# Kernel optimization log

Measured on AMD Instinct MI355X. Metric: run time of the kernel, lower is better.

Reference implementation:

```python
import jax, jax.numpy as jnp
import numpy as np
from functools import partial

B, S, V, H, NH, NKV, M, L = 2, 2048, 51200, 1536, 24, 4, 8960, 8
DH = H // NH  # 64
EPS = 1e-6


def setup_inputs() -> dict:
    key = jax.random.key(0)
    ks = jax.random.split(key, 16)
    sc = 0.02
    w = lambda k, shape: jax.random.normal(k, shape, jnp.float32) * sc
    inp = {
        "input_ids": jax.random.randint(ks[0], (B, S), 0, V),
        "attention_mask": jnp.ones((B, S), jnp.float32),
        "embed": w(ks[1], (V, H)),
        "Wq": w(ks[2], (L, H, H)),          "bq": jnp.zeros((L, H), jnp.float32),
        "Wk": w(ks[3], (L, H, NKV * DH)),   "bk": jnp.zeros((L, NKV * DH), jnp.float32),
        "Wv": w(ks[4], (L, H, NKV * DH)),   "bv": jnp.zeros((L, NKV * DH), jnp.float32),
        "Wo": w(ks[5], (L, H, H)),
        "ln1": jnp.ones((L, H), jnp.float32),
        "ln2": jnp.ones((L, H), jnp.float32),
        "Wg": w(ks[6], (L, H, M)),
        "Wu": w(ks[7], (L, H, M)),
        "Wd": w(ks[8], (L, M, H)),
        "norm_w": jnp.ones((H,), jnp.float32),
        "W1": w(ks[9], (H, H)), "b1": jnp.zeros((H,), jnp.float32),
        "W2": w(ks[10], (H, 1)), "b2": jnp.zeros((1,), jnp.float32),
    }
    inv_freq = 1.0 / (10000.0 ** (jnp.arange(0, DH, 2, dtype=jnp.float32) / DH))
    freqs = jnp.outer(jnp.arange(S, dtype=jnp.float32), inv_freq)  # [S, DH/2]
    emb = jnp.concatenate([freqs, freqs], axis=-1)                 # [S, DH]
    inp["cos"] = jnp.cos(emb)
    inp["sin"] = jnp.sin(emb)
    return inp


def _rms(x, w):
    var = jnp.mean(x.astype(jnp.float32) ** 2, axis=-1, keepdims=True)
    return w * (x * jax.lax.rsqrt(var + EPS)).astype(x.dtype)


def _rotate_half(x):
    x1, x2 = jnp.split(x, 2, axis=-1)
    return jnp.concatenate([-x2, x1], axis=-1)


def _forward(input_ids, attention_mask, embed, Wq, bq, Wk, bk, Wv, bv, Wo,
             ln1, ln2, Wg, Wu, Wd, norm_w, W1, b1, W2, b2, cos, sin):
    scale = 1.0 / np.sqrt(DH)
    b, s = input_ids.shape
    c = cos[None, :s, None, :]  # [1,S,1,DH]
    sn = sin[None, :s, None, :]
    rope = lambda t: t * c + _rotate_half(t) * sn
    mask0 = attention_mask[:, None, None, :] == 0  # [B,1,1,S]

    def block(x, p):
        wq, bq_, wk, bk_, wv, bv_, wo, ln1w, ln2w, wg, wu, wd = p
        h = _rms(x, ln1w)
        q = (h @ wq + bq_).reshape(b, s, NH, DH)
        k = (h @ wk + bk_).reshape(b, s, NKV, DH)
        v = (h @ wv + bv_).reshape(b, s, NKV, DH)
        q, k = rope(q), rope(k)
        k = jnp.repeat(k, NH // NKV, axis=2)  # GQA expand to NH heads
        v = jnp.repeat(v, NH // NKV, axis=2)
        scores = jnp.einsum('bqhd,bkhd->bhqk', q, k) * scale
        scores = jnp.where(mask0, -1e10, scores)
        probs = jax.nn.softmax(scores, axis=-1)  # dropout: eval mode (identity)
        attn = jnp.einsum('bhqk,bkhd->bqhd', probs, v).reshape(b, s, H)
        x = x + attn @ wo
        h = _rms(x, ln2w)
        x = x + (jax.nn.sigmoid(h @ wg) * (h @ wu)) @ wd
        return x, None

    x = embed[input_ids]  # [B,S,H]
    x, _ = jax.lax.scan(block, x, (Wq, bq, Wk, bk, Wv, bv, Wo, ln1, ln2, Wg, Wu, Wd))
    x = _rms(x, norm_w)
    h = jax.nn.gelu(x @ W1 + b1, approximate=False)  # torch nn.GELU default = exact
    return h @ W2 + b2  # [B,S,1]


def reference(input_ids, attention_mask, embed, Wq, bq, Wk, bk, Wv, bv, Wo,
              ln1, ln2, Wg, Wu, Wd, norm_w, W1, b1, W2, b2, cos, sin):
    return _forward(input_ids, attention_mask, embed, Wq, bq, Wk, bk, Wv, bv, Wo,
                    ln1, ln2, Wg, Wu, Wd, norm_w, W1, b1, W2, b2, cos, sin)
```

## Files before the change

kernel.cpp:

```cpp
#include <hip/hip_runtime.h>

typedef float f32x4 __attribute__((ext_vector_type(4)));
typedef short s16x8 __attribute__((ext_vector_type(8)));
typedef unsigned short u16;
typedef unsigned short u16x4 __attribute__((ext_vector_type(4)));
typedef unsigned short u16x8 __attribute__((ext_vector_type(8)));
typedef unsigned int u32x2 __attribute__((ext_vector_type(2)));

__device__ __forceinline__ float bf2f(u16 u){ union{unsigned int i; float f;} v; v.i=((unsigned int)u)<<16; return v.f; }
__device__ __forceinline__ u16 f2bf(float f){ union{float f; unsigned int i;} v; v.f=f; return (u16)((v.i + 0x7FFFu + ((v.i>>16)&1u))>>16); }
__device__ __forceinline__ float aexp2(float x){ float r; asm("v_exp_f32 %0, %1" : "=v"(r) : "v"(x)); return r; }
__device__ __forceinline__ unsigned int cvtpk(float lo, float hi){ unsigned int r; asm("v_cvt_pk_bf16_f32 %0, %1, %2" : "=v"(r) : "v"(lo), "v"(hi)); return r; }

#define LOG2E 1.44269504089f

__device__ __forceinline__ void gld16(const void* gp, void* lp){
  __builtin_amdgcn_global_load_lds((__attribute__((address_space(1))) void*)(void*)gp,
                                   (__attribute__((address_space(3))) void*)lp, 16, 0, 0);
}

__device__ __forceinline__ void job_map(int bid, int gridx, int nrt, int nct, int ksplit,
                                        int SR, int SC, int& rt, int& ct, int& ks){
  int jpx = gridx >> 3;
  int wgid = (bid & 7)*jpx + (bid >> 3);
  int nj1 = nrt*nct;
  ks = wgid / nj1; int rr = wgid - ks*nj1;
  int spc = SR*SC, nstc = nct/SC;
  int st = rr / spc, win = rr - st*spc;
  int str_ = st / nstc, stc = st - str_*nstc;
  int wr = win / SC, wc = win - wr*SC;
  rt = str_*SR + wr;
  ct = stc*SC + wc;
}

__global__ __launch_bounds__(256) void k_embed(const int* __restrict__ ids, const float* __restrict__ emb, float* __restrict__ x){
  int r = blockIdx.x;
  int id = ids[r];
  const f32x4* src = (const f32x4*)(emb + (size_t)id*1536);
  f32x4* dst = (f32x4*)(x + (size_t)r*1536);
  for (int i = threadIdx.x; i < 384; i += 256) dst[i] = src[i];
}

__global__ __launch_bounds__(256) void k_mask(const float* __restrict__ mask, u16* __restrict__ mtab){
  int i = blockIdx.x*256 + threadIdx.x;
  float mv = mask[i];
  mtab[i] = (mv==0.f) ? f2bf(-1.4e9f) : f2bf(-4.f*LOG2E);
}

__global__ __launch_bounds__(256) void k_rms(const float* __restrict__ x, const float* __restrict__ w, u16* __restrict__ h){
  int r = blockIdx.x, tid = threadIdx.x;
  const f32x4* xr = (const f32x4*)(x + (size_t)r*1536);
  f32x4 v0 = xr[tid];
  float ss = v0.x*v0.x + v0.y*v0.y + v0.z*v0.z + v0.w*v0.w;
  f32x4 v1 = {0,0,0,0};
  if (tid < 128){ v1 = xr[256+tid]; ss += v1.x*v1.x + v1.y*v1.y + v1.z*v1.z + v1.w*v1.w; }
  #pragma unroll
  for (int off=32; off; off>>=1) ss += __shfl_xor(ss, off, 64);
  __shared__ float red[4];
  if ((tid&63)==0) red[tid>>6] = ss;
  __syncthreads();
  float tot = red[0]+red[1]+red[2]+red[3];
  float invr = rsqrtf(tot*(1.f/1536.f) + 1e-6f);
  const f32x4* w4 = (const f32x4*)w;
  u16x4* h4 = (u16x4*)(h + (size_t)r*1536);
  {
    f32x4 wv = w4[tid];
    u16x4 o; o.x=f2bf(v0.x*invr*wv.x); o.y=f2bf(v0.y*invr*wv.y); o.z=f2bf(v0.z*invr*wv.z); o.w=f2bf(v0.w*invr*wv.w);
    h4[tid] = o;
  }
  if (tid < 128){
    f32x4 wv = w4[256+tid];
    u16x4 o; o.x=f2bf(v1.x*invr*wv.x); o.y=f2bf(v1.y*invr*wv.y); o.z=f2bf(v1.z*invr*wv.z); o.w=f2bf(v1.w*invr*wv.w);
    h4[256+tid] = o;
  }
}

__global__ __launch_bounds__(256) void k_rms_add(float* __restrict__ x, const float* __restrict__ P, const float* __restrict__ w, u16* __restrict__ h){
  int r = blockIdx.x, tid = threadIdx.x;
  f32x4* xr = (f32x4*)(x + (size_t)r*1536);
  const f32x4* pr = (const f32x4*)(P + (size_t)r*1536);
  f32x4 v0 = xr[tid], p0 = pr[tid];
  v0.x+=p0.x; v0.y+=p0.y; v0.z+=p0.z; v0.w+=p0.w;
  xr[tid] = v0;
  float ss = v0.x*v0.x + v0.y*v0.y + v0.z*v0.z + v0.w*v0.w;
  f32x4 v1 = {0,0,0,0};
  if (tid < 128){
    v1 = xr[256+tid]; f32x4 p1 = pr[256+tid];
    v1.x+=p1.x; v1.y+=p1.y; v1.z+=p1.z; v1.w+=p1.w;
    xr[256+tid] = v1;
    ss += v1.x*v1.x + v1.y*v1.y + v1.z*v1.z + v1.w*v1.w;
  }
  #pragma unroll
  for (int off=32; off; off>>=1) ss += __shfl_xor(ss, off, 64);
  __shared__ float red[4];
  if ((tid&63)==0) red[tid>>6] = ss;
  __syncthreads();
  float tot = red[0]+red[1]+red[2]+red[3];
  float invr = rsqrtf(tot*(1.f/1536.f) + 1e-6f);
  const f32x4* w4 = (const f32x4*)w;
  u16x4* h4 = (u16x4*)(h + (size_t)r*1536);
  {
    f32x4 wv = w4[tid];
    u16x4 o; o.x=f2bf(v0.x*invr*wv.x); o.y=f2bf(v0.y*invr*wv.y); o.z=f2bf(v0.z*invr*wv.z); o.w=f2bf(v0.w*invr*wv.w);
    h4[tid] = o;
  }
  if (tid < 128){
    f32x4 wv = w4[256+tid];
    u16x4 o; o.x=f2bf(v1.x*invr*wv.x); o.y=f2bf(v1.y*invr*wv.y); o.z=f2bf(v1.z*invr*wv.z); o.w=f2bf(v1.w*invr*wv.w);
    h4[256+tid] = o;
  }
}

__device__ __forceinline__ void cvt_tile(const float* src, int K, int N, u16* dst, int k0, int n0, int roff, int mode){
  __shared__ float T[64*72];
  int tid = threadIdx.x;
  #pragma unroll
  for (int j=0;j<4;++j){
    int i = tid + j*256;
    int row = i>>4, nf = i&15;
    f32x4 vv = *(const f32x4*)(src + (size_t)(k0+row)*N + n0 + nf*4);
    *(f32x4*)&T[row*72 + nf*4] = vv;
  }
  __syncthreads();
  #pragma unroll
  for (int j=0;j<2;++j){
    int i = tid + j*256;
    int n = i>>3, kc = i&7;
    u16x8 o;
    #pragma unroll
    for (int m=0;m<8;++m) o[m] = f2bf(T[(kc*8+m)*72 + n]);
    int gn = n0 + n;
    int dr = (mode==0) ? (roff + gn) : (((gn>>4)<<5) + ((mode==2)?16:0) + (gn&15));
    *(u16x8*)(dst + (size_t)dr*K + k0 + kc*8) = o;
  }
}

__global__ __launch_bounds__(256) void k_cvt_layer(
  const float* __restrict__ Wq, const float* __restrict__ Wk, const float* __restrict__ Wv,
  const float* __restrict__ Wo, const float* __restrict__ Wg, const float* __restrict__ Wu,
  const float* __restrict__ Wd, u16* qkvt, u16* wot, u16* gut, u16* wdt)
{
  const float* src; int K, N; u16* dst; int roff=0, mode=0;
  switch (blockIdx.y){
    case 0: src=Wq; K=1536; N=1536; dst=qkvt; break;
    case 1: src=Wk; K=1536; N=256;  dst=qkvt; roff=1536; break;
    case 2: src=Wv; K=1536; N=256;  dst=qkvt; roff=1792; break;
    case 3: src=Wo; K=1536; N=1536; dst=wot;  break;
    case 4: src=Wg; K=1536; N=8960; dst=gut;  mode=1; break;
    case 5: src=Wu; K=1536; N=8960; dst=gut;  mode=2; break;
    default: src=Wd; K=8960; N=1536; dst=wdt; break;
  }
  int ntn = N>>6;
  int nt = (K>>6)*ntn;
  int t = blockIdx.x;
  if (t >= nt) return;
  cvt_tile(src, K, N, dst, (t/ntn)<<6, (t%ntn)<<6, roff, mode);
}

__global__ __launch_bounds__(256) void k_cvt_one(const float* __restrict__ src, u16* __restrict__ dst){
  int t = blockIdx.x;
  cvt_tile(src, 1536, 1536, dst, (t/24)<<6, (t%24)<<6, 0, 0);
}

#define MODE_QKV 0
#define MODE_WO 1
#define MODE_GATEUP 2
#define MODE_DOWN 3
#define MODE_W1 4

template<int MODE>
__global__ __launch_bounds__(256) void k_gemm(
  const u16* __restrict__ A, const u16* __restrict__ Bt, int K,
  int nrt, int nct, int ksplit, int klen, int SR, int SC,
  const float* __restrict__ bq_, const float* __restrict__ bk_, const float* __restrict__ bv_,
  float* __restrict__ xio, float* __restrict__ Pf,
  const float* __restrict__ cosT, const float* __restrict__ sinT,
  u16* __restrict__ o0, u16* __restrict__ o1, u16* __restrict__ o2)
{
  int rt, ct, ks;
  job_map(blockIdx.x, gridDim.x, nrt, nct, ksplit, SR, SC, rt, ct, ks);
  int kbase = ks*klen;
  int nt = klen >> 5;

  __shared__ __align__(16) u16 As[3][4096], Bs[3][4096];
  int tid = threadIdx.x;
  int lane = tid & 63, w = tid >> 6;
  int wr = w >> 1, wc = w & 1;
  int row0 = rt * 128, col0 = ct * 128;
  int l15 = lane & 15, l4 = lane >> 4;
  f32x4 acc[4][4] = {};
  const u16* aBase = A + (size_t)row0*K;
  const u16* bBase = Bt + (size_t)col0*K;
  int rr0 = tid & 127, kb0 = tid >> 7;
  int kb1 = kb0 + 2;

  auto stage = [&](int bf, int kt){
    gld16(aBase + (size_t)rr0*K + kt + kb0*8, &As[bf][tid*8]);
    gld16(bBase + (size_t)rr0*K + kt + kb0*8, &Bs[bf][tid*8]);
    gld16(aBase + (size_t)rr0*K + kt + kb1*8, &As[bf][(256+tid)*8]);
    gld16(bBase + (size_t)rr0*K + kt + kb1*8, &Bs[bf][(256+tid)*8]);
  };
  stage(0, kbase); stage(1, kbase+32);

  int bf = 0;
  for (int t = 0; t < nt; ++t){
    if (t < nt-1) asm volatile("s_waitcnt vmcnt(4)" ::: "memory");
    else          asm volatile("s_waitcnt vmcnt(0)" ::: "memory");
    __builtin_amdgcn_s_barrier();
    __builtin_amdgcn_sched_barrier(0);
    if (t+2 < nt){
      int nb = bf+2; if (nb >= 3) nb -= 3;
      stage(nb, kbase + (t+2)*32);
    }
    const u16* Ab = As[bf];
    const u16* Bb = Bs[bf];
    s16x8 af[4], bf_[4];
    #pragma unroll
    for (int i=0;i<4;++i) af[i]  = *(const s16x8*)&Ab[((l4<<7) + wr*64 + i*16 + l15)*8];
    #pragma unroll
    for (int jj=0;jj<4;++jj) bf_[jj] = *(const s16x8*)&Bb[((l4<<7) + wc*64 + jj*16 + l15)*8];
    __builtin_amdgcn_s_setprio(1);
    #pragma unroll
    for (int i=0;i<4;++i)
      #pragma unroll
      for (int jj=0;jj<4;++jj)
        acc[i][jj] = __builtin_amdgcn_mfma_f32_16x16x32_bf16(af[i], bf_[jj], acc[i][jj], 0, 0, 0);
    __builtin_amdgcn_s_setprio(0);
    if (++bf == 3) bf = 0;
  }

  #pragma unroll
  for (int i=0;i<4;++i)
    #pragma unroll
    for (int jj=0;jj<4;++jj)
      #pragma unroll
      for (int r=0;r<4;++r){
        int row = row0 + wr*64 + i*16 + l4*4 + r;
        int c   = col0 + wc*64 + jj*16 + l15;
        float v = acc[i][jj][r];
        if constexpr (MODE == MODE_QKV){
          int b = row >> 11, s = row & 2047;
          if (c < 1536){
            int d = c & 63, hd = c >> 6;
            float vv = v + bq_[c];
            float pv = acc[i][jj^2][r] + bq_[c^32];
            float cv = cosT[s*64+d], sv = sinT[s*64+d];
            float sgn = (d<32) ? -1.f : 1.f;
            float o = (vv*cv + sgn*pv*sv)*(0.125f*LOG2E);
            o0[(size_t)(b*24+hd)*131072 + (size_t)(s>>6)*4096
               + (s&63)*64 + (((d>>3)^(s&7))<<3) + (d&7)] = f2bf(o);
          } else if (c < 1792){
            int c2 = c - 1536, d = c2 & 63, kv = c2 >> 6;
            float vv = v + bk_[c2];
            float pv = acc[i][jj^2][r] + bk_[c2^32];
            float cv = cosT[s*64+d], sv = sinT[s*64+d];
            float sgn = (d<32) ? -1.f : 1.f;
            float o = vv*cv + sgn*pv*sv;
            o1[(size_t)(b*4+kv)*131072 + (size_t)(s>>6)*4096
               + (s&63)*64 + (((d>>3)^(s&7))<<3) + (d&7)] = f2bf(o);
          } else {
            int c2 = c - 1792, d = c2 & 63, kv = c2 >> 6;
            float vv = v + bv_[c2];
            o2[(size_t)(b*4+kv)*131072 + (size_t)(s>>6)*4096
               + d*64 + ((((s>>3)&7)^(d&7))<<3) + (s&7)] = f2bf(vv);
          }
        } else if constexpr (MODE == MODE_WO){
          xio[(size_t)row*1536 + c] += v;
        } else if constexpr (MODE == MODE_W1){
          v += bq_[c];
          float ge = 0.5f * v * (1.f + erff(v * 0.70710678118f));
          o0[(size_t)row*1536 + c] = f2bf(ge);
        }
      }
}

template<int MODE>
__global__ __launch_bounds__(512,2) void k_gemm256(
  const u16* __restrict__ A, const u16* __restrict__ Bt, int K,
  int nrt, int nct, int ksplit, int klen, int SR, int SC,
  float* __restrict__ xio, float* __restrict__ Pf, u16* __restrict__ o0)
{
  int rt, ct, ks;
  job_map(blockIdx.x, gridDim.x, nrt, nct, ksplit, SR, SC, rt, ct, ks);

  __shared__ __align__(16) u16 lds[2][2][16384];
  int tid = threadIdx.x;
  int lane = tid & 63, wid = tid >> 6;
  int wm = wid >> 2, wn = wid & 3;
  int l15 = lane & 15, l4 = lane >> 4;
  int lsw = l15 & 7;
  int row0 = rt*256, col0 = ct*256;
  int kbase = ks*klen*64;

  const u16* aB = A  + (size_t)row0*K + kbase;
  const u16* bB = Bt + (size_t)col0*K + kbase;
  int rsub = tid >> 3;
  int gsw  = (lane & 7) ^ ((lane >> 3) & 7);

  f32x4 acc[8][4] = {};

  auto sgA = [&](int bf, int kt, int c){
    gld16(aB + (size_t)(c*64 + rsub)*K + kt*64 + gsw*8, &lds[bf][0][(c*512+tid)*8]);
  };
  auto sgB = [&](int bf, int kt, int c){
    gld16(bB + (size_t)(c*64 + rsub)*K + kt*64 + gsw*8, &lds[bf][1][(c*512+tid)*8]);
  };

  sgB(0,0,0); sgB(0,0,1); sgB(0,0,2); sgB(0,0,3);
  sgA(0,0,0); sgA(0,0,2); sgA(0,0,1); sgA(0,0,3);

  for (int t = 0; t < klen; ++t){
    int b = t & 1, nb = b ^ 1;
    bool hn = (t+1 < klen);
    const u16* Ab = lds[b][0];
    const u16* Bb = lds[b][1];
    s16x8 bfr[4][2];

    asm volatile("s_waitcnt vmcnt(2)" ::: "memory");
    __builtin_amdgcn_s_barrier();
    __builtin_amdgcn_sched_barrier(0);
    {
      s16x8 af[2][2];
      #pragma unroll
      for (int ii=0;ii<2;++ii)
        #pragma unroll
        for (int ksu=0;ksu<2;++ksu)
          af[ii][ksu] = *(const s16x8*)&Ab[(wm*128 + ii*16 + l15)*64 + (((ksu*4+l4)^lsw)<<3)];
      #pragma unroll
      for (int j=0;j<4;++j)
        #pragma unroll
        for (int ksu=0;ksu<2;++ksu)
          bfr[j][ksu] = *(const s16x8*)&Bb[(wn*64 + j*16 + l15)*64 + (((ksu*4+l4)^lsw)<<3)];
      if (hn){ sgB(nb, t+1, 0); sgB(nb, t+1, 1); }
      asm volatile("s_waitcnt lgkmcnt(0)" ::: "memory");
      __builtin_amdgcn_sched_barrier(0);
      __builtin_amdgcn_s_setprio(1);
      #pragma unroll
      for (int ii=0;ii<2;++ii)
        #pragma unroll
        for (int j=0;j<4;++j)
          #pragma unroll
          for (int ksu=0;ksu<2;++ksu)
            acc[ii][j] = __builtin_amdgcn_mfma_f32_16x16x32_bf16(af[ii][ksu], bfr[j][ksu], acc[ii][j], 0,0,0);
      __builtin_amdgcn_s_setprio(0);
      __builtin_amdgcn_s_barrier();
    }
    {
      s16x8 af[2][2];
      #pragma unroll
      for (int ii=0;ii<2;++ii)
        #pragma unroll
        for (int ksu=0;ksu<2;++ksu)
          af[ii][ksu] = *(const s16x8*)&Ab[(wm*128 + 32 + ii*16 + l15)*64 + (((ksu*4+l4)^lsw)<<3)];
      if (hn){ sgB(nb, t+1, 2); sgB(nb, t+1, 3); }
      asm volatile("s_waitcnt lgkmcnt(0)" ::: "memory");
      __builtin_amdgcn_sched_barrier(0);
      __builtin_amdgcn_s_setprio(1);
      #pragma unroll
      for (int ii=0;ii<2;++ii)
        #pragma unroll
        for (int j=0;j<4;++j)
          #pragma unroll
          for (int ksu=0;ksu<2;++ksu)
            acc[2+ii][j] = __builtin_amdgcn_mfma_f32_16x16x32_bf16(af[ii][ksu], bfr[j][ksu], acc[2+ii][j], 0,0,0);
      __builtin_amdgcn_s_setprio(0);
      __builtin_amdgcn_s_barrier();
    }
    if (hn) asm volatile("s_waitcnt vmcnt(4)" ::: "memory");
    else    asm volatile("s_waitcnt vmcnt(0)" ::: "memory");
    __builtin_amdgcn_s_barrier();
    __builtin_amdgcn_sched_barrier(0);
    {
      s16x8 af[2][2];
      #pragma unroll
      for (int ii=0;ii<2;++ii)
        #pragma unroll
        for (int ksu=0;ksu<2;++ksu)
          af[ii][ksu] = *(const s16x8*)&Ab[(wm*128 + 64 + ii*16 + l15)*64 + (((ksu*4+l4)^lsw)<<3)];
      if (hn){ sgA(nb, t+1, 0); sgA(nb, t+1, 2); }
      asm volatile("s_waitcnt lgkmcnt(0)" ::: "memory");
      __builtin_amdgcn_sched_barrier(0);
      __builtin_amdgcn_s_setprio(1);
      #pragma unroll
      for (int ii=0;ii<2;++ii)
        #pragma unroll
        for (int j=0;j<4;++j)
          #pragma unroll
          for (int ksu=0;ksu<2;++ksu)
            acc[4+ii][j] = __builtin_amdgcn_mfma_f32_16x16x32_bf16(af[ii][ksu], bfr[j][ksu], acc[4+ii][j], 0,0,0);
      __builtin_amdgcn_s_setprio(0);
      __builtin_amdgcn_s_barrier();
    }
    {
      s16x8 af[2][2];
      #pragma unroll
      for (int ii=0;ii<2;++ii)
        #pragma unroll
        for (int ksu=0;ksu<2;++ksu)
          af[ii][ksu] = *(const s16x8*)&Ab[(wm*128 + 96 + ii*16 + l15)*64 + (((ksu*4+l4)^lsw)<<3)];
      if (hn){ sgA(nb, t+1, 1); sgA(nb, t+1, 3); }
      asm volatile("s_waitcnt lgkmcnt(0)" ::: "memory");
      __builtin_amdgcn_sched_barrier(0);
      __builtin_amdgcn_s_setprio(1);
      #pragma unroll
      for (int ii=0;ii<2;++ii)
        #pragma unroll
        for (int j=0;j<4;++j)
          #pragma unroll
          for (int ksu=0;ksu<2;++ksu)
            acc[6+ii][j] = __builtin_amdgcn_mfma_f32_16x16x32_bf16(af[ii][ksu], bfr[j][ksu], acc[6+ii][j], 0,0,0);
      __builtin_amdgcn_s_setprio(0);
      __builtin_amdgcn_s_barrier();
    }
  }

  if constexpr (MODE == MODE_GATEUP){
    #pragma unroll
    for (int i=0;i<8;++i)
      #pragma unroll
      for (int j2=0;j2<4;j2+=2)
        #pragma unroll
        for (int r=0;r<4;++r){
          int row = row0 + wm*128 + i*16 + l4*4 + r;
          int cp  = col0 + wn*64 + j2*16 + l15;
          float gv = acc[i][j2][r], uv = acc[i][j2+1][r];
          float sg = 1.f/(1.f + __expf(-gv));
          int n = ((cp>>5)<<4) + (cp&15);
          o0[(size_t)row*8960 + n] = f2bf(sg*uv);
        }
  } else {
    #pragma unroll
    for (int i=0;i<8;++i)
      #pragma unroll
      for (int j=0;j<4;++j)
        #pragma unroll
        for (int r=0;r<4;++r){
          int row = row0 + wm*128 + i*16 + l4*4 + r;
          int c   = col0 + wn*64 + j*16 + l15;
          float v = acc[i][j][r];
          if (ks == 0) Pf[(size_t)row*1536 + c] = v;
          else         xio[(size_t)row*1536 + c] += v;
        }
  }
}

__global__ __launch_bounds__(256) void k_attn(
  const u16* __restrict__ q, const u16* __restrict__ k, const u16* __restrict__ v,
  const u16* __restrict__ mtab, u16* __restrict__ attn)
{
  __shared__ __align__(16) u16 Qs[8192];
  __shared__ __align__(16) u16 Kd[2][4096];
  __shared__ __align__(16) u16 Vd[2][4096];
  int tid = threadIdx.x;
  int lane = tid & 63, w = tid >> 6;
  int qb = blockIdx.x;
  int bh = blockIdx.y;
  int b = bh / 24, hh = bh % 24, kv = hh / 6;
  int l15 = lane & 15, l4 = lane >> 4;
  int sw = l15 & 7;

  const u16* qhead = q + ((size_t)(b*24 + hh))*131072 + qb*8192;
  const u16* khead = k + ((size_t)(b*4  + kv))*131072;
  const u16* vhead = v + ((size_t)(b*4  + kv))*131072;
  const u16* mrow = mtab + b*2048;

  gld16(qhead + tid*8,        &Qs[tid*8]);
  gld16(qhead + (256+tid)*8,  &Qs[(256+tid)*8]);
  gld16(qhead + (512+tid)*8,  &Qs[(512+tid)*8]);
  gld16(qhead + (768+tid)*8,  &Qs[(768+tid)*8]);

  auto stage = [&](int bf, int kt){
    gld16(khead + kt*4096 + tid*8,       &Kd[bf][tid*8]);
    gld16(khead + kt*4096 + (256+tid)*8, &Kd[bf][(256+tid)*8]);
    gld16(vhead + kt*4096 + tid*8,       &Vd[bf][tid*8]);
    gld16(vhead + kt*4096 + (256+tid)*8, &Vd[bf][(256+tid)*8]);
  };
  stage(0, 0);

  s16x8 aq[2][2];
  f32x4 oacc[2][4] = {};
  float lsum[2] = {0.f, 0.f};
  u16* Pw = &Qs[w*2048];

  for (int t = 0; t < 32; ++t){
    asm volatile("s_waitcnt vmcnt(0)" ::: "memory");
    __builtin_amdgcn_s_barrier();
    __builtin_amdgcn_sched_barrier(0);
    if (t == 0){
      #pragma unroll
      for (int qa=0; qa<2; ++qa){
        int qrow = w*32 + qa*16 + l15;
        aq[qa][0] = *(const s16x8*)&Qs[qrow*64 + (( l4    ^ sw)<<3)];
        aq[qa][1] = *(const s16x8*)&Qs[qrow*64 + (((4+l4) ^ sw)<<3)];
      }
    }
    if (t+1 < 32) stage((t+1)&1, t+1);
    const u16* Kb = Kd[t&1];
    const u16* Vb = Vd[t&1];
    f32x4 sk[2][4] = {};
    __builtin_amdgcn_s_setprio(1);
    #pragma unroll
    for (int kn=0; kn<4; ++kn){
      int krow = kn*16 + l15;
      s16x8 a0 = *(const s16x8*)&Kb[krow*64 + (( l4    ^ sw)<<3)];
      s16x8 a1 = *(const s16x8*)&Kb[krow*64 + (((4+l4) ^ sw)<<3)];
      #pragma unroll
      for (int qa=0; qa<2; ++qa){
        sk[qa][kn] = __builtin_amdgcn_mfma_f32_16x16x32_bf16(a0, aq[qa][0], sk[qa][kn], 0,0,0);
        sk[qa][kn] = __builtin_amdgcn_mfma_f32_16x16x32_bf16(a1, aq[qa][1], sk[qa][kn], 0,0,0);
      }
    }
    __builtin_amdgcn_s_setprio(0);
    #pragma unroll
    for (int kn=0; kn<4; ++kn){
      u16x4 mv = *(const u16x4*)&mrow[t*64 + kn*16 + l4*4];
      #pragma unroll
      for (int qa=0; qa<2; ++qa){
        float p0 = aexp2(sk[qa][kn][0] + bf2f(mv.x));
        float p1 = aexp2(sk[qa][kn][1] + bf2f(mv.y));
        float p2 = aexp2(sk[qa][kn][2] + bf2f(mv.z));
        float p3 = aexp2(sk[qa][kn][3] + bf2f(mv.w));
        lsum[qa] += (p0 + p1) + (p2 + p3);
        u32x2 pk; pk.x = cvtpk(p0, p1); pk.y = cvtpk(p2, p3);
        int g = kn*2 + (l4>>1);
        *(u32x2*)&Pw[(qa*16 + l15)*64 + ((g ^ sw)<<3) + (l4&1)*4] = pk;
      }
    }
    __builtin_amdgcn_s_setprio(1);
    #pragma unroll
    for (int ksu=0; ksu<2; ++ksu){
      s16x8 bv[4];
      #pragma unroll
      for (int dg=0; dg<4; ++dg)
        bv[dg] = *(const s16x8*)&Vb[(dg*16+l15)*64 + (((ksu*4+l4) ^ sw)<<3)];
      #pragma unroll
      for (int qa=0; qa<2; ++qa){
        s16x8 ap = *(const s16x8*)&Pw[(qa*16 + l15)*64 + (((ksu*4+l4) ^ sw)<<3)];
        #pragma unroll
        for (int dg=0; dg<4; ++dg)
          oacc[qa][dg] = __builtin_amdgcn_mfma_f32_16x16x32_bf16(ap, bv[dg], oacc[qa][dg], 0,0,0);
      }
    }
    __builtin_amdgcn_s_setprio(0);
  }
  #pragma unroll
  for (int qa=0; qa<2; ++qa){
    float t2 = lsum[qa];
    t2 += __shfl_xor(t2, 16, 64);
    t2 += __shfl_xor(t2, 32, 64);
    float invq[4];
    #pragma unroll
    for (int r=0;r<4;++r) invq[r] = 1.f / __shfl(t2, l4*4 + r, 64);
    #pragma unroll
    for (int dg=0;dg<4;++dg)
      #pragma unroll
      for (int r=0;r<4;++r){
        int token = b*2048 + qb*128 + w*32 + qa*16 + l4*4 + r;
        int col = hh*64 + dg*16 + l15;
        attn[(size_t)token*1536 + col] = f2bf(oacc[qa][dg][r] * invq[r]);
      }
  }
}

__global__ __launch_bounds__(256) void k_gemv(const u16* __restrict__ h2, const float* __restrict__ W2, const float* __restrict__ b2, float* __restrict__ out){
  int tid = threadIdx.x, lane = tid & 63, w = tid >> 6;
  int r = blockIdx.x*4 + w;
  const u16* hr = h2 + (size_t)r*1536;
  float s = 0.f;
  #pragma unroll
  for (int i=0;i<24;++i){ int c = lane + i*64; s += bf2f(hr[c]) * W2[c]; }
  #pragma unroll
  for (int off=32; off; off>>=1) s += __shfl_xor(s, off, 64);
  if (lane == 0) out[r] = s + b2[0];
}

extern "C" void kernel_launch(void* const* d_in, const int* in_sizes, int n_in,
                              void* d_out, int out_size, void* d_ws, size_t ws_size,
                              hipStream_t stream)
{
  const int*   ids   = (const int*)d_in[0];
  const float* mask  = (const float*)d_in[1];
  const float* embed = (const float*)d_in[2];
  const float* Wq    = (const float*)d_in[3];
  const float* bq    = (const float*)d_in[4];
  const float* Wk    = (const float*)d_in[5];
  const float* bk    = (const float*)d_in[6];
  const float* Wv    = (const float*)d_in[7];
  const float* bv    = (const float*)d_in[8];
  const float* Wo    = (const float*)d_in[9];
  const float* ln1   = (const float*)d_in[10];
  const float* ln2   = (const float*)d_in[11];
  const float* Wg    = (const float*)d_in[12];
  const float* Wu    = (const float*)d_in[13];
  const float* Wd    = (const float*)d_in[14];
  const float* nw    = (const float*)d_in[15];
  const float* W1    = (const float*)d_in[16];
  const float* b1    = (const float*)d_in[17];
  const float* W2    = (const float*)d_in[18];
  const float* b2    = (const float*)d_in[19];
  const float* cosT  = (const float*)d_in[20];
  const float* sinT  = (const float*)d_in[21];

  char* ws = (char*)d_ws;
  float* x   = (float*)(ws + 0);
  u16* h     = (u16*)(ws + 25165824);
  u16* qb_   = (u16*)(ws + 37748736);
  u16* kb_   = (u16*)(ws + 50331648);
  u16* vb_   = (u16*)(ws + 52428800);
  u16* attn  = (u16*)(ws + 54525952);
  u16* g     = (u16*)(ws + 67108864);
  u16* qkvt  = (u16*)(ws + 140509184);
  u16* wot   = (u16*)(ws + 146800640);
  u16* gut   = (u16*)(ws + 151519232);
  u16* wdt   = (u16*)(ws + 206569472);
  u16* mtab  = (u16*)(ws + 234094592);
  float* Pf  = (float*)(ws + 37748736);
  (void)in_sizes; (void)n_in; (void)out_size; (void)ws_size;

  k_embed<<<4096, 256, 0, stream>>>(ids, embed, x);
  k_mask<<<16, 256, 0, stream>>>(mask, mtab);
  for (int l = 0; l < 8; ++l){
    k_cvt_layer<<<dim3(3360,7), 256, 0, stream>>>(
      Wq + (size_t)l*1536*1536, Wk + (size_t)l*1536*256, Wv + (size_t)l*1536*256,
      Wo + (size_t)l*1536*1536, Wg + (size_t)l*1536*8960, Wu + (size_t)l*1536*8960,
      Wd + (size_t)l*8960*1536, qkvt, wot, gut, wdt);
    if (l == 0) k_rms<<<4096, 256, 0, stream>>>(x, ln1, h);
    else        k_rms_add<<<4096, 256, 0, stream>>>(x, Pf, ln1 + l*1536, h);
    k_gemm<MODE_QKV><<<512, 256, 0, stream>>>(h, qkvt, 1536, 32, 16, 1, 1536, 8, 4,
        bq + l*1536, bk + l*256, bv + l*256, nullptr, nullptr, cosT, sinT, qb_, kb_, vb_);
    k_attn<<<dim3(16,48), 256, 0, stream>>>(qb_, kb_, vb_, mtab, attn);
    k_gemm<MODE_WO><<<384, 256, 0, stream>>>(attn, wot, 1536, 32, 12, 1, 1536, 8, 4,
        nullptr, nullptr, nullptr, x, nullptr, nullptr, nullptr, nullptr, nullptr, nullptr);
    k_rms<<<4096, 256, 0, stream>>>(x, ln2 + l*1536, h);
    k_gemm256<MODE_GATEUP><<<1120, 512, 0, stream>>>(h, gut, 1536, 16, 70, 1, 24, 8, 10,
        nullptr, nullptr, g);
    k_gemm256<MODE_DOWN><<<192, 512, 0, stream>>>(g, wdt, 8960, 16, 6, 2, 70, 4, 6,
        x, Pf, nullptr);
  }
  k_cvt_one<<<576, 256, 0, stream>>>(W1, wot);
  k_rms_add<<<4096, 256, 0, stream>>>(x, Pf, nw, h);
  k_gemm<MODE_W1><<<384, 256, 0, stream>>>(h, wot, 1536, 32, 12, 1, 1536, 8, 4,
      b1, nullptr, nullptr, nullptr, nullptr, nullptr, nullptr, attn, nullptr, nullptr);
  k_gemv<<<1024, 256, 0, stream>>>(attn, W2, b2, (float*)d_out);
}
```

Measured before the change: 5.128 ms.

## Batch rows per block in embed and RMSNorm kernels, store mask as fp32

The embedding gather now copies 8 rows per block, and the RMSNorm kernels handle 2 rows per 512-thread block, so far fewer, larger workgroups are launched. The mask table moves from bf16 to fp32, which removes the bf16-to-float conversion in the attention softmax loop at the cost of twice as many bytes per mask load. These kernels are small and memory-bound next to the GEMMs and attention, so the overall effect should be minor.

```diff
diff --git a/kernel.cpp b/kernel.cpp
--- a/kernel.cpp
+++ b/kernel.cpp
@@ -34,80 +34,92 @@
 }
 
 __global__ __launch_bounds__(256) void k_embed(const int* __restrict__ ids, const float* __restrict__ emb, float* __restrict__ x){
-  int r = blockIdx.x;
-  int id = ids[r];
-  const f32x4* src = (const f32x4*)(emb + (size_t)id*1536);
-  f32x4* dst = (f32x4*)(x + (size_t)r*1536);
-  for (int i = threadIdx.x; i < 384; i += 256) dst[i] = src[i];
-}
-
-__global__ __launch_bounds__(256) void k_mask(const float* __restrict__ mask, u16* __restrict__ mtab){
+  __shared__ int sid[8];
+  int tid = threadIdx.x;
+  int r0 = blockIdx.x*8;
+  if (tid < 8) sid[tid] = ids[r0+tid];
+  __syncthreads();
+  #pragma unroll
+  for (int j=0;j<12;++j){
+    int i = j*256 + tid;
+    int row = i/384, col = i - row*384;
+    const f32x4* src = (const f32x4*)(emb + (size_t)sid[row]*1536);
+    f32x4* dst = (f32x4*)(x + (size_t)(r0+row)*1536);
+    dst[col] = src[col];
+  }
+}
+
+__global__ __launch_bounds__(256) void k_mask(const float* __restrict__ mask, float* __restrict__ mtab){
   int i = blockIdx.x*256 + threadIdx.x;
   float mv = mask[i];
-  mtab[i] = (mv==0.f) ? f2bf(-1.4e9f) : f2bf(-4.f*LOG2E);
-}
-
-__global__ __launch_bounds__(256) void k_rms(const float* __restrict__ x, const float* __restrict__ w, u16* __restrict__ h){
-  int r = blockIdx.x, tid = threadIdx.x;
+  mtab[i] = (mv==0.f) ? -1.4e9f : (-4.f*LOG2E);
+}
+
+__global__ __launch_bounds__(512) void k_rms(const float* __restrict__ x, const float* __restrict__ w, u16* __restrict__ h){
+  int tid = threadIdx.x;
+  int half = tid >> 8, t2 = tid & 255;
+  int r = blockIdx.x*2 + half;
   const f32x4* xr = (const f32x4*)(x + (size_t)r*1536);
-  f32x4 v0 = xr[tid];
+  f32x4 v0 = xr[t2];
   float ss = v0.x*v0.x + v0.y*v0.y + v0.z*v0.z + v0.w*v0.w;
   f32x4 v1 = {0,0,0,0};
-  if (tid < 128){ v1 = xr[256+tid]; ss += v1.x*v1.x + v1.y*v1.y + v1.z*v1.z + v1.w*v1.w; }
+  if (t2 < 128){ v1 = xr[256+t2]; ss += v1.x*v1.x + v1.y*v1.y + v1.z*v1.z + v1.w*v1.w; }
   #pragma unroll
   for (int off=32; off; off>>=1) ss += __shfl_xor(ss, off, 64);
-  __shared__ float red[4];
+  __shared__ float red[8];
   if ((tid&63)==0) red[tid>>6] = ss;
   __syncthreads();
-  float tot = red[0]+red[1]+red[2]+red[3];
+  float tot = red[half*4+0]+red[half*4+1]+red[half*4+2]+red[half*4+3];
   float invr = rsqrtf(tot*(1.f/1536.f) + 1e-6f);
   const f32x4* w4 = (const f32x4*)w;
   u16x4* h4 = (u16x4*)(h + (size_t)r*1536);
   {
-    f32x4 wv = w4[tid];
+    f32x4 wv = w4[t2];
     u16x4 o; o.x=f2bf(v0.x*invr*wv.x); o.y=f2bf(v0.y*invr*wv.y); o.z=f2bf(v0.z*invr*wv.z); o.w=f2bf(v0.w*invr*wv.w);
-    h4[tid] = o;
-  }
-  if (tid < 128){
-    f32x4 wv = w4[256+tid];
+    h4[t2] = o;
+  }
+  if (t2 < 128){
+    f32x4 wv = w4[256+t2];
     u16x4 o; o.x=f2bf(v1.x*invr*wv.x); o.y=f2bf(v1.y*invr*wv.y); o.z=f2bf(v1.z*invr*wv.z); o.w=f2bf(v1.w*invr*wv.w);
-    h4[256+tid] = o;
-  }
-}
-
-__global__ __launch_bounds__(256) void k_rms_add(float* __restrict__ x, const float* __restrict__ P, const float* __restrict__ w, u16* __restrict__ h){
-  int r = blockIdx.x, tid = threadIdx.x;
+    h4[256+t2] = o;
+  }
+}
+
+__global__ __launch_bounds__(512) void k_rms_add(float* __restrict__ x, const float* __restrict__ P, const float* __restrict__ w, u16* __restrict__ h){
+  int tid = threadIdx.x;
+  int half = tid >> 8, t2 = tid & 255;
+  int r = blockIdx.x*2 + half;
   f32x4* xr = (f32x4*)(x + (size_t)r*1536);
   const f32x4* pr = (const f32x4*)(P + (size_t)r*1536);
-  f32x4 v0 = xr[tid], p0 = pr[tid];
+  f32x4 v0 = xr[t2], p0 = pr[t2];
   v0.x+=p0.x; v0.y+=p0.y; v0.z+=p0.z; v0.w+=p0.w;
-  xr[tid] = v0;
+  xr[t2] = v0;
   float ss = v0.x*v0.x + v0.y*v0.y + v0.z*v0.z + v0.w*v0.w;
   f32x4 v1 = {0,0,0,0};
-  if (tid < 128){
-    v1 = xr[256+tid]; f32x4 p1 = pr[256+tid];
+  if (t2 < 128){
+    v1 = xr[256+t2]; f32x4 p1 = pr[256+t2];
     v1.x+=p1.x; v1.y+=p1.y; v1.z+=p1.z; v1.w+=p1.w;
-    xr[256+tid] = v1;
+    xr[256+t2] = v1;
     ss += v1.x*v1.x + v1.y*v1.y + v1.z*v1.z + v1.w*v1.w;
   }
   #pragma unroll
   for (int off=32; off; off>>=1) ss += __shfl_xor(ss, off, 64);
-  __shared__ float red[4];
+  __shared__ float red[8];
   if ((tid&63)==0) red[tid>>6] = ss;
   __syncthreads();
-  float tot = red[0]+red[1]+red[2]+red[3];
+  float tot = red[half*4+0]+red[half*4+1]+red[half*4+2]+red[half*4+3];
   float invr = rsqrtf(tot*(1.f/1536.f) + 1e-6f);
   const f32x4* w4 = (const f32x4*)w;
   u16x4* h4 = (u16x4*)(h + (size_t)r*1536);
   {
-    f32x4 wv = w4[tid];
+    f32x4 wv = w4[t2];
     u16x4 o; o.x=f2bf(v0.x*invr*wv.x); o.y=f2bf(v0.y*invr*wv.y); o.z=f2bf(v0.z*invr*wv.z); o.w=f2bf(v0.w*invr*wv.w);
-    h4[tid] = o;
-  }
-  if (tid < 128){
-    f32x4 wv = w4[256+tid];
+    h4[t2] = o;
+  }
+  if (t2 < 128){
+    f32x4 wv = w4[256+t2];
     u16x4 o; o.x=f2bf(v1.x*invr*wv.x); o.y=f2bf(v1.y*invr*wv.y); o.z=f2bf(v1.z*invr*wv.z); o.w=f2bf(v1.w*invr*wv.w);
-    h4[256+tid] = o;
+    h4[256+t2] = o;
   }
 }
 
@@ -446,7 +458,7 @@
 
 __global__ __launch_bounds__(256) void k_attn(
   const u16* __restrict__ q, const u16* __restrict__ k, const u16* __restrict__ v,
-  const u16* __restrict__ mtab, u16* __restrict__ attn)
+  const float* __restrict__ mtab, u16* __restrict__ attn)
 {
   __shared__ __align__(16) u16 Qs[8192];
   __shared__ __align__(16) u16 Kd[2][4096];
@@ -462,7 +474,7 @@
   const u16* qhead = q + ((size_t)(b*24 + hh))*131072 + qb*8192;
   const u16* khead = k + ((size_t)(b*4  + kv))*131072;
   const u16* vhead = v + ((size_t)(b*4  + kv))*131072;
-  const u16* mrow = mtab + b*2048;
+  const float* mrow = mtab + b*2048;
 
   gld16(qhead + tid*8,        &Qs[tid*8]);
   gld16(qhead + (256+tid)*8,  &Qs[(256+tid)*8]);
@@ -513,13 +525,13 @@
     __builtin_amdgcn_s_setprio(0);
     #pragma unroll
     for (int kn=0; kn<4; ++kn){
-      u16x4 mv = *(const u16x4*)&mrow[t*64 + kn*16 + l4*4];
+      f32x4 mv = *(const f32x4*)&mrow[t*64 + kn*16 + l4*4];
       #pragma unroll
       for (int qa=0; qa<2; ++qa){
-        float p0 = aexp2(sk[qa][kn][0] + bf2f(mv.x));
-        float p1 = aexp2(sk[qa][kn][1] + bf2f(mv.y));
-        float p2 = aexp2(sk[qa][kn][2] + bf2f(mv.z));
-        float p3 = aexp2(sk[qa][kn][3] + bf2f(mv.w));
+        float p0 = aexp2(sk[qa][kn][0] + mv.x);
+        float p1 = aexp2(sk[qa][kn][1] + mv.y);
+        float p2 = aexp2(sk[qa][kn][2] + mv.z);
+        float p3 = aexp2(sk[qa][kn][3] + mv.w);
         lsum[qa] += (p0 + p1) + (p2 + p3);
         u32x2 pk; pk.x = cvtpk(p0, p1); pk.y = cvtpk(p2, p3);
         int g = kn*2 + (l4>>1);
@@ -613,32 +625,32 @@
   u16* wot   = (u16*)(ws + 146800640);
   u16* gut   = (u16*)(ws + 151519232);
   u16* wdt   = (u16*)(ws + 206569472);
-  u16* mtab  = (u16*)(ws + 234094592);
+  float* mtab = (float*)(ws + 234094592);
   float* Pf  = (float*)(ws + 37748736);
   (void)in_sizes; (void)n_in; (void)out_size; (void)ws_size;
 
-  k_embed<<<4096, 256, 0, stream>>>(ids, embed, x);
+  k_embed<<<512, 256, 0, stream>>>(ids, embed, x);
   k_mask<<<16, 256, 0, stream>>>(mask, mtab);
   for (int l = 0; l < 8; ++l){
     k_cvt_layer<<<dim3(3360,7), 256, 0, stream>>>(
       Wq + (size_t)l*1536*1536, Wk + (size_t)l*1536*256, Wv + (size_t)l*1536*256,
       Wo + (size_t)l*1536*1536, Wg + (size_t)l*1536*8960, Wu + (size_t)l*1536*8960,
       Wd + (size_t)l*8960*1536, qkvt, wot, gut, wdt);
-    if (l == 0) k_rms<<<4096, 256, 0, stream>>>(x, ln1, h);
-    else        k_rms_add<<<4096, 256, 0, stream>>>(x, Pf, ln1 + l*1536, h);
+    if (l == 0) k_rms<<<2048, 512, 0, stream>>>(x, ln1, h);
+    else        k_rms_add<<<2048, 512, 0, stream>>>(x, Pf, ln1 + l*1536, h);
     k_gemm<MODE_QKV><<<512, 256, 0, stream>>>(h, qkvt, 1536, 32, 16, 1, 1536, 8, 4,
         bq + l*1536, bk + l*256, bv + l*256, nullptr, nullptr, cosT, sinT, qb_, kb_, vb_);
     k_attn<<<dim3(16,48), 256, 0, stream>>>(qb_, kb_, vb_, mtab, attn);
     k_gemm<MODE_WO><<<384, 256, 0, stream>>>(attn, wot, 1536, 32, 12, 1, 1536, 8, 4,
         nullptr, nullptr, nullptr, x, nullptr, nullptr, nullptr, nullptr, nullptr, nullptr);
-    k_rms<<<4096, 256, 0, stream>>>(x, ln2 + l*1536, h);
+    k_rms<<<2048, 512, 0, stream>>>(x, ln2 + l*1536, h);
     k_gemm256<MODE_GATEUP><<<1120, 512, 0, stream>>>(h, gut, 1536, 16, 70, 1, 24, 8, 10,
         nullptr, nullptr, g);
     k_gemm256<MODE_DOWN><<<192, 512, 0, stream>>>(g, wdt, 8960, 16, 6, 2, 70, 4, 6,
         x, Pf, nullptr);
   }
   k_cvt_one<<<576, 256, 0, stream>>>(W1, wot);
-  k_rms_add<<<4096, 256, 0, stream>>>(x, Pf, nw, h);
+  k_rms_add<<<2048, 512, 0, stream>>>(x, Pf, nw, h);
   k_gemm<MODE_W1><<<384, 256, 0, stream>>>(h, wot, 1536, 32, 12, 1, 1536, 8, 4,
       b1, nullptr, nullptr, nullptr, nullptr, nullptr, nullptr, attn, nullptr, nullptr);
   k_gemv<<<1024, 256, 0, stream>>>(attn, W2, b2, (float*)d_out);
```

Result: no change. 5.131 ms (+0.1%).
